# Optimization experiments

Hardware: AMD Instinct MI355X
Metric: run time of the kernel (lower is better)

The kernel has to match this reference:

```python
import jax, jax.numpy as jnp
import numpy as np

T, B, X, H, Y, D = 512, 64, 64, 1024, 64, 2


def setup_inputs() -> dict:
    key = jax.random.key(0)
    ks = jax.random.split(key, 13)
    s = 0.02  # weight init scale
    return {
        "x": jax.random.normal(ks[0], (T, B, X), dtype=jnp.float32),
        "enc_w": jax.random.normal(ks[1], (H, X), dtype=jnp.float32) * s,
        "enc_b": jax.random.normal(ks[2], (H,), dtype=jnp.float32) * s,
        "w_ih": jax.random.normal(ks[3], (D, 3 * H, H), dtype=jnp.float32) * s,
        "w_hh": jax.random.normal(ks[4], (D, 3 * H, H), dtype=jnp.float32) * s,
        "b_ih": jax.random.normal(ks[5], (D, 3 * H), dtype=jnp.float32) * s,
        "b_hh": jax.random.normal(ks[6], (D, 3 * H), dtype=jnp.float32) * s,
        "dec_w": jax.random.normal(ks[7], (H, H), dtype=jnp.float32) * s,
        "dec_b": jax.random.normal(ks[8], (H,), dtype=jnp.float32) * s,
        "exp_w": jax.random.normal(ks[9], (Y, H), dtype=jnp.float32) * s,
        "exp_b": jax.random.normal(ks[10], (Y,), dtype=jnp.float32) * s,
        "log_w": jax.random.normal(ks[11], (Y, H), dtype=jnp.float32) * s,
        "log_b": jax.random.normal(ks[12], (Y,), dtype=jnp.float32) * s,
    }


def _gru_cell(x, h, wih, whh, bih, bhh):
    # PyTorch GRUCell semantics
    gi = x @ wih.T + bih  # [B, 3H]
    gh = h @ whh.T + bhh  # [B, 3H]
    i_r, i_z, i_n = jnp.split(gi, 3, axis=-1)
    h_r, h_z, h_n = jnp.split(gh, 3, axis=-1)
    r = jax.nn.sigmoid(i_r + h_r)
    z = jax.nn.sigmoid(i_z + h_z)
    n = jnp.tanh(i_n + r * h_n)
    return (1.0 - z) * n + z * h


def reference(x, enc_w, enc_b, w_ih, w_hh, b_ih, b_hh, dec_w, dec_b,
              exp_w, exp_b, log_w, log_b):
    depth = w_ih.shape[0]
    batch = x.shape[1]
    h0 = jnp.zeros((depth, batch, w_hh.shape[-1]), dtype=x.dtype)

    def step(h_states, x_t):
        rnn_in = jnp.tanh(x_t @ enc_w.T + enc_b)  # encoder
        new_h = []
        for i in range(depth):  # small fixed stack of structurally distinct cells
            h = _gru_cell(rnn_in, h_states[i], w_ih[i], w_hh[i], b_ih[i], b_hh[i])
            new_h.append(h)
            rnn_in = h
        rnn_out = jnp.tanh(rnn_in @ dec_w.T + dec_b)  # decoder
        mean = rnn_out @ exp_w.T + exp_b
        var = jnp.exp(rnn_out @ log_w.T + log_b)
        return jnp.stack(new_h), (mean, var)

    _, (time_mean, time_var) = jax.lax.scan(step, h0, x)
    return time_mean, time_var  # each [T, B, Y]
```

## Files before the change

kernel.cpp:

```cpp
#include <hip/hip_runtime.h>
#include <hip/hip_bf16.h>
#include <cstdint>

#define T_STEPS 512
#define BATCH   64
#define XDIM    64
#define HDIM    1024
#define YDIM    64
#define BH      (BATCH * HDIM)
#define RING_D  32

#define WBLK_BYTES   98304
#define COMBO_BYTES  24576
#define TL1_OFF      16384

typedef unsigned short ushort_t;
typedef uint32_t u32;
typedef unsigned long long u64;
typedef __attribute__((ext_vector_type(8))) short short8;
typedef __attribute__((ext_vector_type(4))) float f32x4;

__device__ __forceinline__ u32 f2bf_u(float x) {
  u32 u = __float_as_uint(x);
  return (u + 0x7fffu + ((u >> 16) & 1u)) >> 16;
}
__device__ __forceinline__ ushort_t f2bf(float x) { return (ushort_t)f2bf_u(x); }

__device__ __forceinline__ float sigm(float x) { return 1.0f / (1.0f + expf(-x)); }

__device__ __forceinline__ void st_sc32(u32* p, u32 v) {
  __hip_atomic_store(p, v, __ATOMIC_RELAXED, __HIP_MEMORY_SCOPE_AGENT);
}
__device__ __forceinline__ u32 ld_sc32(const u32* p) {
  return __hip_atomic_load((u32*)p, __ATOMIC_RELAXED, __HIP_MEMORY_SCOPE_AGENT);
}

__global__ __launch_bounds__(256) void enc_kernel(
    const float* __restrict__ x, const float* __restrict__ enc_w,
    const float* __restrict__ enc_b, ushort_t* __restrict__ enc_out)
{
  __shared__ float wlds[64 * 65];
  const int lane = threadIdx.x & 63;
  const int wv   = threadIdx.x >> 6;
  const int cb = blockIdx.x & 15;
  const int rb = blockIdx.x >> 4;
  const int j  = cb * 64 + lane;
  const int r0 = rb * 16 + wv * 4;

  const float* wsrc = enc_w + (size_t)cb * 64 * XDIM;
  for (int i = threadIdx.x; i < 4096; i += 256)
    wlds[(i >> 6) * 65 + (i & 63)] = wsrc[i];
  __syncthreads();

  const float* xr = x + (size_t)r0 * XDIM;
  float acc[4] = {0.f, 0.f, 0.f, 0.f};
#pragma unroll
  for (int k = 0; k < XDIM; k += 4) {
    const float w0 = wlds[lane * 65 + k];
    const float w1 = wlds[lane * 65 + k + 1];
    const float w2 = wlds[lane * 65 + k + 2];
    const float w3 = wlds[lane * 65 + k + 3];
#pragma unroll
    for (int rr = 0; rr < 4; ++rr) {
      const float* xp = xr + rr * XDIM + k;
      acc[rr] = fmaf(xp[3], w3, fmaf(xp[2], w2, fmaf(xp[1], w1, fmaf(xp[0], w0, acc[rr]))));
    }
  }
  const float b = enc_b[j];
#pragma unroll
  for (int rr = 0; rr < 4; ++rr)
    enc_out[(size_t)(r0 + rr) * HDIM + j] = f2bf(tanhf(acc[rr] + b));
}

__global__ __launch_bounds__(256) void wprep_kernel(
    const float* __restrict__ w_ih, const float* __restrict__ w_hh,
    ushort_t* __restrict__ wfrag)
{
  const int lane = threadIdx.x & 63;
  const int wv   = threadIdx.x >> 6;
  const int c    = blockIdx.x * 4 + wv;
  const int ko = c & 15;
  const int tl = (c >> 4) & 1;
  const int c2 = (c >> 5) & 3;
  const int bid = c >> 7;
  const int g = c2 >> 1, kh = c2 & 1;
  const int layer = bid >> 7;
  const int j0 = (bid & 127) * 8;
  const float* wsrc = (g ? w_hh : w_ih) + (size_t)layer * 3 * HDIM * HDIM;

  if (tl == 0) {
    const int col = lane & 15, kgrp = lane >> 4;
    const int k = kh * 512 + ko * 32 + kgrp * 8;
    const int row = (col < 8) ? (j0 + col) : (HDIM + j0 + col - 8);
    const float* src = wsrc + (size_t)row * HDIM + k;
    short8 v;
#pragma unroll
    for (int e = 0; e < 8; ++e) v[e] = (short)f2bf(src[e]);
    const size_t byte = (size_t)bid * WBLK_BYTES + c2 * COMBO_BYTES + ko * 1024 + lane * 16;
    *(short8*)((char*)wfrag + byte) = v;
  } else if (lane < 32) {
    const int kgrp = lane >> 3, col = lane & 7;
    const int k = kh * 512 + ko * 32 + kgrp * 8;
    const int row = 2 * HDIM + j0 + col;
    const float* src = wsrc + (size_t)row * HDIM + k;
    short8 v;
#pragma unroll
    for (int e = 0; e < 8; ++e) v[e] = (short)f2bf(src[e]);
    const size_t byte = (size_t)bid * WBLK_BYTES + c2 * COMBO_BYTES + TL1_OFF + ko * 512 + lane * 16;
    *(short8*)((char*)wfrag + byte) = v;
  }
}

__global__ __launch_bounds__(256) void wprep2_kernel(
    const float* __restrict__ dec_w, const float* __restrict__ exp_w,
    const float* __restrict__ log_w,
    ushort_t* __restrict__ dwfrag, ushort_t* __restrict__ hwfrag)
{
  const int lane = threadIdx.x & 63;
  const int wv   = threadIdx.x >> 6;
  const int c    = blockIdx.x * 4 + wv;
  short8 v;
  if (c < 2048) {
    const int nt = c >> 5, kc = c & 31;
    const int row = nt * 16 + (lane & 15);
    const int k   = kc * 32 + (lane >> 4) * 8;
    const float* src = dec_w + (size_t)row * HDIM + k;
#pragma unroll
    for (int e = 0; e < 8; ++e) v[e] = (short)f2bf(src[e]);
    *(short8*)(dwfrag + (size_t)c * 512 + lane * 8) = v;
  } else {
    const int c2 = c - 2048;
    const int nt = c2 >> 5, kc = c2 & 31;
    const int row = nt * 16 + (lane & 15);
    const int k   = kc * 32 + (lane >> 4) * 8;
    const float* src = (row < 64) ? (exp_w + (size_t)row * HDIM + k)
                                  : (log_w + (size_t)(row - 64) * HDIM + k);
#pragma unroll
    for (int e = 0; e < 8; ++e) v[e] = (short)f2bf(src[e]);
    *(short8*)(hwfrag + (size_t)c2 * 512 + lane * 8) = v;
  }
}

__device__ __forceinline__ void group_bar(u32* flags, u32* rel, int gbid,
                                          bool leader, u32 tag) {
  const int tid = threadIdx.x;
  __syncthreads();
  if (tid == 0) st_sc32(flags + (size_t)gbid * 64, tag);
  if (leader) {
    if (tid < 128) {
      u32* fp = flags + (size_t)tid * 64;
      while (ld_sc32(fp) < tag) __builtin_amdgcn_s_sleep(1);
    }
    __syncthreads();
    if (tid == 0) st_sc32(rel, tag);
  } else {
    if (tid == 0) {
      while (ld_sc32(rel) < tag) __builtin_amdgcn_s_sleep(1);
    }
    __syncthreads();
  }
}

__global__ __launch_bounds__(512, 1) void rnn_persist(
    const ushort_t* __restrict__ ench1,
    const ushort_t* __restrict__ wfrag,
    const float* __restrict__ b_ih, const float* __restrict__ b_hh,
    ushort_t* __restrict__ h0ring,
    ushort_t* __restrict__ h1ring,
    ushort_t* __restrict__ h1_all,
    u32* __restrict__ l0_flags, u32* __restrict__ l1_flags,
    u32* __restrict__ l0_rel,   u32* __restrict__ l1_rel)
{
  extern __shared__ char smem[];
  float* lds_part = (float*)(smem + WBLK_BYTES);

  const int tid  = threadIdx.x;
  const int lane = tid & 63;
  const int wid  = tid >> 6;
  const int bid  = blockIdx.x;
  const int layer = bid >> 7;
  const int j0    = (bid & 127) * 8;
  const int mp = wid & 1, g = (wid >> 1) & 1, kh = wid >> 2;
  const int col = lane & 15, kgrp = lane >> 4;
  const bool isL1 = (layer == 1);
  const int gbid = bid & 127;
  const bool leader = (gbid == 0);

  {
    const uint4* src = (const uint4*)((const char*)wfrag + (size_t)bid * WBLK_BYTES);
    uint4* dst = (uint4*)smem;
#pragma unroll 4
    for (int i = tid; i < WBLK_BYTES / 16; i += 512) dst[i] = src[i];
  }

  const int c2 = g * 2 + kh;
  const char* w0 = smem + c2 * COMBO_BYTES + lane * 16;
  const char* w1 = smem + c2 * COMBO_BYTES + TL1_OFF + (kgrp * 8 + (col & 7)) * 16;

  float bA = 0.f, bB = 0.f, bC = 0.f;
  {
    const float* bi = b_ih + layer * 3 * HDIM;
    const float* bh = b_hh + layer * 3 * HDIM;
    if (col < 8) {
      const int j = j0 + col;
      bA = bi[j] + bh[j];
      bB = bi[2 * HDIM + j];
      bC = bh[2 * HDIM + j];
    } else {
      const int j = j0 + col - 8;
      bA = bi[HDIM + j] + bh[HDIM + j];
    }
  }

  f32x4 hp = {0.f, 0.f, 0.f, 0.f};

  __syncthreads();

  for (int i = 0; i < T_STEPS; ++i) {
    if (isL1) {
      if (tid == 0) {
        while (ld_sc32(l0_rel) < (u32)(i + 1)) __builtin_amdgcn_s_sleep(1);
      }
    } else if (i >= RING_D) {
      if (tid == 0) {
        while (ld_sc32(l1_rel) < (u32)(i - RING_D + 1)) __builtin_amdgcn_s_sleep(1);
      }
    }
    __syncthreads();

    const ushort_t* A1 = isL1 ? (h0ring + (size_t)(i & (RING_D - 1)) * BH)
                              : (ench1 + (size_t)i * BH);
    const ushort_t* A2 = isL1 ? (h1ring + (size_t)((i - 1) & (RING_D - 1)) * BH)
                              : (h0ring + (size_t)((i - 1) & (RING_D - 1)) * BH);
    const ushort_t* A = g ? A2 : A1;
    const ushort_t* Arow0 = A + (size_t)(mp * 32 + col) * HDIM + kh * 512 + kgrp * 8;
    const ushort_t* Arow1 = Arow0 + 16 * HDIM;

    f32x4 acc00 = {0,0,0,0}, acc01 = {0,0,0,0}, acc10 = {0,0,0,0}, acc11 = {0,0,0,0};
#pragma unroll
    for (int ko = 0; ko < 16; ++ko) {
      const short8 a0 = *(const short8*)(Arow0 + ko * 32);
      const short8 a1 = *(const short8*)(Arow1 + ko * 32);
      const short8 b0 = *(const short8*)(w0 + ko * 1024);
      const short8 b1 = *(const short8*)(w1 + ko * 512);
      acc00 = __builtin_amdgcn_mfma_f32_16x16x32_bf16(a0, b0, acc00, 0, 0, 0);
      acc01 = __builtin_amdgcn_mfma_f32_16x16x32_bf16(a0, b1, acc01, 0, 0, 0);
      acc10 = __builtin_amdgcn_mfma_f32_16x16x32_bf16(a1, b0, acc10, 0, 0, 0);
      acc11 = __builtin_amdgcn_mfma_f32_16x16x32_bf16(a1, b1, acc11, 0, 0, 0);
    }
    const int base = (wid * 4) * 256 + lane * 4;
    *(f32x4*)&lds_part[base      ] = acc00;
    *(f32x4*)&lds_part[base + 256] = acc01;
    *(f32x4*)&lds_part[base + 512] = acc10;
    *(f32x4*)&lds_part[base + 768] = acc11;

    __syncthreads();

    if (wid < 4) {
      const int m = wid, mpe = m >> 1, ime = m & 1;
      const int i00 = ((0 * 4 + 0 * 2 + mpe) * 4 + ime * 2);
      const int i01 = ((1 * 4 + 0 * 2 + mpe) * 4 + ime * 2);
      const int i10 = ((0 * 4 + 1 * 2 + mpe) * 4 + ime * 2);
      const int i11 = ((1 * 4 + 1 * 2 + mpe) * 4 + ime * 2);
      const int lo = lane * 4;
      f32x4 girz = *(f32x4*)&lds_part[i00 * 256 + lo] + *(f32x4*)&lds_part[i01 * 256 + lo];
      f32x4 gin  = *(f32x4*)&lds_part[(i00 + 1) * 256 + lo] + *(f32x4*)&lds_part[(i01 + 1) * 256 + lo];
      f32x4 ghrz = *(f32x4*)&lds_part[i10 * 256 + lo] + *(f32x4*)&lds_part[i11 * 256 + lo];
      f32x4 ghn  = *(f32x4*)&lds_part[(i10 + 1) * 256 + lo] + *(f32x4*)&lds_part[(i11 + 1) * 256 + lo];

      ushort_t* hdst = isL1 ? (h1ring + (size_t)(i & (RING_D - 1)) * BH)
                            : (h0ring + (size_t)(i & (RING_D - 1)) * BH);
      ushort_t* hall = isL1 ? (h1_all + (size_t)i * BH) : (ushort_t*)0;

#pragma unroll
      for (int e = 0; e < 4; ++e) {
        const float rz = sigm(girz[e] + ghrz[e] + bA);
        const float nv = tanhf(gin[e] + bB + rz * (ghn[e] + bC));
        const float zv = __shfl_xor(rz, 8);
        const int b = m * 16 + kgrp * 4 + e;
        float h = 0.f;
        if (col < 8) {
          h = (1.f - zv) * nv + zv * hp[e];
          hp[e] = h;
        }
        const u32 hb = f2bf_u(h);
        const u32 pb = (u32)__shfl_xor((int)hb, 1);
        if (col < 8 && (col & 1) == 0) {
          const u32 pack = hb | (pb << 16);
          st_sc32((u32*)(hdst + b * HDIM + j0 + col), pack);
          if (hall) st_sc32((u32*)(hall + b * HDIM + j0 + col), pack);
        }
      }
    }

    if (isL1) group_bar(l1_flags, l1_rel, gbid, leader, (u32)(i + 1));
    else      group_bar(l0_flags, l0_rel, gbid, leader, (u32)(i + 1));
  }
}

#define AST 1032
__global__ __launch_bounds__(512, 1) void dechead_kernel(
    const ushort_t* __restrict__ h1_all,
    const ushort_t* __restrict__ dwfrag, const ushort_t* __restrict__ hwfrag,
    const float* __restrict__ dec_b, const float* __restrict__ exp_b,
    const float* __restrict__ log_b, float* __restrict__ out)
{
  extern __shared__ char smem2[];
  ushort_t* Alds = (ushort_t*)smem2;
  ushort_t* Rlds = Alds + 32 * AST;

  const int tid  = threadIdx.x;
  const int lane = tid & 63;
  const int wv   = tid >> 6;
  const int base = blockIdx.x * 32;

  {
    const uint4* src = (const uint4*)(h1_all + (size_t)base * HDIM);
#pragma unroll
    for (int ii = 0; ii < 8; ++ii) {
      const int idx = ii * 512 + tid;
      const int row = idx >> 7;
      const int k   = (idx & 127) * 8;
      *(uint4*)(Alds + row * AST + k) = src[idx];
    }
  }
  __syncthreads();

  f32x4 acc[8][2];
#pragma unroll
  for (int t = 0; t < 8; ++t) { acc[t][0] = (f32x4){0,0,0,0}; acc[t][1] = (f32x4){0,0,0,0}; }

  const int r0 = lane & 15, kg = lane >> 4;
  const int nt0 = wv * 8;
#pragma unroll 1
  for (int t = 0; t < 8; ++t) {
    const ushort_t* bsrc = dwfrag + (size_t)(nt0 + t) * 32 * 512 + lane * 8;
    f32x4 c0 = acc[t][0], c1 = acc[t][1];
#pragma unroll
    for (int kc = 0; kc < 32; ++kc) {
      const short8 b  = *(const short8*)(bsrc + kc * 512);
      const short8 a0 = *(const short8*)(Alds + r0 * AST + kc * 32 + kg * 8);
      const short8 a1 = *(const short8*)(Alds + (16 + r0) * AST + kc * 32 + kg * 8);
      c0 = __builtin_amdgcn_mfma_f32_16x16x32_bf16(a0, b, c0, 0, 0, 0);
      c1 = __builtin_amdgcn_mfma_f32_16x16x32_bf16(a1, b, c1, 0, 0, 0);
    }
    acc[t][0] = c0; acc[t][1] = c1;
  }

#pragma unroll
  for (int t = 0; t < 8; ++t) {
    const int colc = (nt0 + t) * 16 + r0;
    const float db = dec_b[colc];
#pragma unroll
    for (int m = 0; m < 2; ++m) {
      const f32x4 v = acc[t][m];
#pragma unroll
      for (int e = 0; e < 4; ++e) {
        const int row = m * 16 + kg * 4 + e;
        Rlds[row * AST + colc] = (ushort_t)f2bf_u(tanhf(v[e] + db));
      }
    }
  }
  __syncthreads();

  f32x4 h0a = {0,0,0,0}, h1a = {0,0,0,0};
  {
    const ushort_t* bsrc = hwfrag + (size_t)wv * 32 * 512 + lane * 8;
#pragma unroll
    for (int kc = 0; kc < 32; ++kc) {
      const short8 b  = *(const short8*)(bsrc + kc * 512);
      const short8 a0 = *(const short8*)(Rlds + r0 * AST + kc * 32 + kg * 8);
      const short8 a1 = *(const short8*)(Rlds + (16 + r0) * AST + kc * 32 + kg * 8);
      h0a = __builtin_amdgcn_mfma_f32_16x16x32_bf16(a0, b, h0a, 0, 0, 0);
      h1a = __builtin_amdgcn_mfma_f32_16x16x32_bf16(a1, b, h1a, 0, 0, 0);
    }
  }
  const int y = wv * 16 + r0;
  if (wv < 4) {
    const float eb = exp_b[y];
#pragma unroll
    for (int m = 0; m < 2; ++m) {
      const f32x4 v = (m == 0) ? h0a : h1a;
#pragma unroll
      for (int e = 0; e < 4; ++e) {
        const int row = m * 16 + kg * 4 + e;
        out[(size_t)(base + row) * YDIM + y] = v[e] + eb;
      }
    }
  } else {
    const int yv = y - 64;
    const float lb = log_b[yv];
#pragma unroll
    for (int m = 0; m < 2; ++m) {
      const f32x4 v = (m == 0) ? h0a : h1a;
#pragma unroll
      for (int e = 0; e < 4; ++e) {
        const int row = m * 16 + kg * 4 + e;
        out[(size_t)(T_STEPS * BATCH * YDIM) + (size_t)(base + row) * YDIM + yv] = expf(v[e] + lb);
      }
    }
  }
}

extern "C" void kernel_launch(void* const* d_in, const int* in_sizes, int n_in,
                              void* d_out, int out_size, void* d_ws, size_t ws_size,
                              hipStream_t stream) {
  (void)in_sizes; (void)n_in; (void)out_size; (void)ws_size;
  const float* x     = (const float*)d_in[0];
  const float* enc_w = (const float*)d_in[1];
  const float* enc_b = (const float*)d_in[2];
  const float* w_ih  = (const float*)d_in[3];
  const float* w_hh  = (const float*)d_in[4];
  const float* b_ih  = (const float*)d_in[5];
  const float* b_hh  = (const float*)d_in[6];
  const float* dec_w = (const float*)d_in[7];
  const float* dec_b = (const float*)d_in[8];
  const float* exp_w = (const float*)d_in[9];
  const float* exp_b = (const float*)d_in[10];
  const float* log_w = (const float*)d_in[11];
  const float* log_b = (const float*)d_in[12];
  float* out = (float*)d_out;

  char* ws = (char*)d_ws;
  u32*      l0f     = (u32*)ws;
  u32*      l1f     = (u32*)(ws + 32768);
  u32*      l0r     = (u32*)(ws + 65536);
  u32*      l1r     = (u32*)(ws + 65792);
  ushort_t* wfrag   = (ushort_t*)(ws + 2097152);
  ushort_t* h0ring  = (ushort_t*)(ws + 27262976);
  ushort_t* h1ring  = (ushort_t*)(ws + 31457280);
  ushort_t* ench1   = (ushort_t*)(ws + 35651584);
  ushort_t* dwfrag  = (ushort_t*)(ws + 102760448);
  ushort_t* hwfrag  = (ushort_t*)(ws + 104857600);

  hipMemsetAsync(ws, 0, 66048, stream);
  hipMemsetAsync(ws + 27262976, 0, 8388608, stream);

  enc_kernel<<<32768, 256, 0, stream>>>(x, enc_w, enc_b, ench1);
  wprep_kernel<<<8192, 256, 0, stream>>>(w_ih, w_hh, wfrag);
  wprep2_kernel<<<576, 256, 0, stream>>>(dec_w, exp_w, log_w, dwfrag, hwfrag);

  {
    static int lds_opted = 0;
    if (!lds_opted) {
      hipFuncSetAttribute((const void*)rnn_persist,
                          hipFuncAttributeMaxDynamicSharedMemorySize, 131072);
      hipFuncSetAttribute((const void*)dechead_kernel,
                          hipFuncAttributeMaxDynamicSharedMemorySize, 2 * 32 * AST * 2);
      lds_opted = 1;
    }
    void* args[11];
    args[0]  = (void*)&ench1;
    args[1]  = (void*)&wfrag;
    args[2]  = (void*)&b_ih;
    args[3]  = (void*)&b_hh;
    args[4]  = (void*)&h0ring;
    args[5]  = (void*)&h1ring;
    args[6]  = (void*)&ench1;
    args[7]  = (void*)&l0f;
    args[8]  = (void*)&l1f;
    args[9]  = (void*)&l0r;
    args[10] = (void*)&l1r;
    hipLaunchCooperativeKernel((const void*)rnn_persist, dim3(256), dim3(512),
                               args, 131072, stream);
  }

  dechead_kernel<<<1024, 512, 2 * 32 * AST * 2, stream>>>(
      ench1, dwfrag, hwfrag, dec_b, exp_b, log_b, out);
}
```

Measured before the change: 5.984 ms.

## Replace leader-based group barrier with distributed flag polling and prefetch A early

Removes the two-level leader/release barrier. Each block now publishes a packed per-step flag, and consumers poll all 128 producer flags directly with 128-bit sc1 loads spread over 32 threads. The input-projection operand (g==0, which does not depend on the previous step) is loaded into registers before waiting on the recurrence flags, so that load overlaps the synchronization wait. The K loop is split into halves gated by explicit vmcnt waits. This shortens the critical path per timestep at the cost of more polling traffic, a large register array (32 uint4), and reliance on inline asm and relaxed memory ordering.

```diff
diff --git a/kernel.cpp b/kernel.cpp
--- a/kernel.cpp
+++ b/kernel.cpp
@@ -20,6 +20,8 @@
 typedef __attribute__((ext_vector_type(8))) short short8;
 typedef __attribute__((ext_vector_type(4))) float f32x4;
 
+union U4S8 { uint4 u; short8 s; };
+
 __device__ __forceinline__ u32 f2bf_u(float x) {
   u32 u = __float_as_uint(x);
   return (u + 0x7fffu + ((u >> 16) & 1u)) >> 16;
@@ -31,8 +33,22 @@
 __device__ __forceinline__ void st_sc32(u32* p, u32 v) {
   __hip_atomic_store(p, v, __ATOMIC_RELAXED, __HIP_MEMORY_SCOPE_AGENT);
 }
-__device__ __forceinline__ u32 ld_sc32(const u32* p) {
-  return __hip_atomic_load((u32*)p, __ATOMIC_RELAXED, __HIP_MEMORY_SCOPE_AGENT);
+
+__device__ __forceinline__ uint4 ld_g128(const ushort_t* p) {
+  uint4 r;
+  asm volatile("global_load_dwordx4 %0, %1, off" : "=v"(r) : "v"(p));
+  return r;
+}
+
+__device__ __forceinline__ int flags_ok(const u32* p, u32 tag) {
+  uint4 f;
+  asm volatile("global_load_dwordx4 %0, %1, off sc1\n\ts_waitcnt vmcnt(0)"
+               : "=v"(f) : "v"(p) : "memory");
+  return (f.x >= tag) && (f.y >= tag) && (f.z >= tag) && (f.w >= tag);
+}
+__device__ __forceinline__ void poll4(const u32* flags, int t, u32 tag) {
+  const u32* p = flags + 4 * t;
+  while (!flags_ok(p, tag)) __builtin_amdgcn_s_sleep(1);
 }
 
 __global__ __launch_bounds__(256) void enc_kernel(
@@ -141,26 +157,6 @@
   }
 }
 
-__device__ __forceinline__ void group_bar(u32* flags, u32* rel, int gbid,
-                                          bool leader, u32 tag) {
-  const int tid = threadIdx.x;
-  __syncthreads();
-  if (tid == 0) st_sc32(flags + (size_t)gbid * 64, tag);
-  if (leader) {
-    if (tid < 128) {
-      u32* fp = flags + (size_t)tid * 64;
-      while (ld_sc32(fp) < tag) __builtin_amdgcn_s_sleep(1);
-    }
-    __syncthreads();
-    if (tid == 0) st_sc32(rel, tag);
-  } else {
-    if (tid == 0) {
-      while (ld_sc32(rel) < tag) __builtin_amdgcn_s_sleep(1);
-    }
-    __syncthreads();
-  }
-}
-
 __global__ __launch_bounds__(512, 1) void rnn_persist(
     const ushort_t* __restrict__ ench1,
     const ushort_t* __restrict__ wfrag,
@@ -168,8 +164,7 @@
     ushort_t* __restrict__ h0ring,
     ushort_t* __restrict__ h1ring,
     ushort_t* __restrict__ h1_all,
-    u32* __restrict__ l0_flags, u32* __restrict__ l1_flags,
-    u32* __restrict__ l0_rel,   u32* __restrict__ l1_rel)
+    u32* __restrict__ l0_flags, u32* __restrict__ l1_flags)
 {
   extern __shared__ char smem[];
   float* lds_part = (float*)(smem + WBLK_BYTES);
@@ -184,7 +179,7 @@
   const int col = lane & 15, kgrp = lane >> 4;
   const bool isL1 = (layer == 1);
   const int gbid = bid & 127;
-  const bool leader = (gbid == 0);
+  u32* ownf = isL1 ? l1_flags : l0_flags;
 
   {
     const uint4* src = (const uint4*)((const char*)wfrag + (size_t)bid * WBLK_BYTES);
@@ -218,15 +213,9 @@
 
   for (int i = 0; i < T_STEPS; ++i) {
     if (isL1) {
-      if (tid == 0) {
-        while (ld_sc32(l0_rel) < (u32)(i + 1)) __builtin_amdgcn_s_sleep(1);
-      }
-    } else if (i >= RING_D) {
-      if (tid == 0) {
-        while (ld_sc32(l1_rel) < (u32)(i - RING_D + 1)) __builtin_amdgcn_s_sleep(1);
-      }
-    }
-    __syncthreads();
+      if (tid < 32) poll4(l0_flags, tid, (u32)(i + 1));
+      __syncthreads();
+    }
 
     const ushort_t* A1 = isL1 ? (h0ring + (size_t)(i & (RING_D - 1)) * BH)
                               : (ench1 + (size_t)i * BH);
@@ -236,18 +225,55 @@
     const ushort_t* Arow0 = A + (size_t)(mp * 32 + col) * HDIM + kh * 512 + kgrp * 8;
     const ushort_t* Arow1 = Arow0 + 16 * HDIM;
 
+    uint4 areg[32];
+    if (g == 0) {
+#pragma unroll
+      for (int ko = 0; ko < 16; ++ko) {
+        areg[2 * ko]     = ld_g128(Arow0 + ko * 32);
+        areg[2 * ko + 1] = ld_g128(Arow1 + ko * 32);
+      }
+    }
+
+    if (tid < 32) {
+      poll4(ownf, tid, (u32)i);
+      if (!isL1 && i >= RING_D) poll4(l1_flags, tid, (u32)(i - RING_D + 1));
+    }
+    __syncthreads();
+
+    if (g == 1) {
+#pragma unroll
+      for (int ko = 0; ko < 16; ++ko) {
+        areg[2 * ko]     = ld_g128(Arow0 + ko * 32);
+        areg[2 * ko + 1] = ld_g128(Arow1 + ko * 32);
+      }
+    }
+
     f32x4 acc00 = {0,0,0,0}, acc01 = {0,0,0,0}, acc10 = {0,0,0,0}, acc11 = {0,0,0,0};
-#pragma unroll
-    for (int ko = 0; ko < 16; ++ko) {
-      const short8 a0 = *(const short8*)(Arow0 + ko * 32);
-      const short8 a1 = *(const short8*)(Arow1 + ko * 32);
+    asm volatile("s_waitcnt vmcnt(16)" ::: "memory");
+    __builtin_amdgcn_sched_barrier(0);
+#pragma unroll
+    for (int ko = 0; ko < 8; ++ko) {
       const short8 b0 = *(const short8*)(w0 + ko * 1024);
       const short8 b1 = *(const short8*)(w1 + ko * 512);
-      acc00 = __builtin_amdgcn_mfma_f32_16x16x32_bf16(a0, b0, acc00, 0, 0, 0);
-      acc01 = __builtin_amdgcn_mfma_f32_16x16x32_bf16(a0, b1, acc01, 0, 0, 0);
-      acc10 = __builtin_amdgcn_mfma_f32_16x16x32_bf16(a1, b0, acc10, 0, 0, 0);
-      acc11 = __builtin_amdgcn_mfma_f32_16x16x32_bf16(a1, b1, acc11, 0, 0, 0);
-    }
+      U4S8 a0, a1; a0.u = areg[2 * ko]; a1.u = areg[2 * ko + 1];
+      acc00 = __builtin_amdgcn_mfma_f32_16x16x32_bf16(a0.s, b0, acc00, 0, 0, 0);
+      acc01 = __builtin_amdgcn_mfma_f32_16x16x32_bf16(a0.s, b1, acc01, 0, 0, 0);
+      acc10 = __builtin_amdgcn_mfma_f32_16x16x32_bf16(a1.s, b0, acc10, 0, 0, 0);
+      acc11 = __builtin_amdgcn_mfma_f32_16x16x32_bf16(a1.s, b1, acc11, 0, 0, 0);
+    }
+    asm volatile("s_waitcnt vmcnt(0)" ::: "memory");
+    __builtin_amdgcn_sched_barrier(0);
+#pragma unroll
+    for (int ko = 8; ko < 16; ++ko) {
+      const short8 b0 = *(const short8*)(w0 + ko * 1024);
+      const short8 b1 = *(const short8*)(w1 + ko * 512);
+      U4S8 a0, a1; a0.u = areg[2 * ko]; a1.u = areg[2 * ko + 1];
+      acc00 = __builtin_amdgcn_mfma_f32_16x16x32_bf16(a0.s, b0, acc00, 0, 0, 0);
+      acc01 = __builtin_amdgcn_mfma_f32_16x16x32_bf16(a0.s, b1, acc01, 0, 0, 0);
+      acc10 = __builtin_amdgcn_mfma_f32_16x16x32_bf16(a1.s, b0, acc10, 0, 0, 0);
+      acc11 = __builtin_amdgcn_mfma_f32_16x16x32_bf16(a1.s, b1, acc11, 0, 0, 0);
+    }
+
     const int base = (wid * 4) * 256 + lane * 4;
     *(f32x4*)&lds_part[base      ] = acc00;
     *(f32x4*)&lds_part[base + 256] = acc01;
@@ -293,8 +319,8 @@
       }
     }
 
-    if (isL1) group_bar(l1_flags, l1_rel, gbid, leader, (u32)(i + 1));
-    else      group_bar(l0_flags, l0_rel, gbid, leader, (u32)(i + 1));
+    __syncthreads();
+    if (tid == 0) st_sc32(ownf + gbid, (u32)(i + 1));
   }
 }
 
@@ -423,9 +449,7 @@
 
   char* ws = (char*)d_ws;
   u32*      l0f     = (u32*)ws;
-  u32*      l1f     = (u32*)(ws + 32768);
-  u32*      l0r     = (u32*)(ws + 65536);
-  u32*      l1r     = (u32*)(ws + 65792);
+  u32*      l1f     = (u32*)(ws + 4096);
   ushort_t* wfrag   = (ushort_t*)(ws + 2097152);
   ushort_t* h0ring  = (ushort_t*)(ws + 27262976);
   ushort_t* h1ring  = (ushort_t*)(ws + 31457280);
@@ -433,7 +457,7 @@
   ushort_t* dwfrag  = (ushort_t*)(ws + 102760448);
   ushort_t* hwfrag  = (ushort_t*)(ws + 104857600);
 
-  hipMemsetAsync(ws, 0, 66048, stream);
+  hipMemsetAsync(ws, 0, 8192, stream);
   hipMemsetAsync(ws + 27262976, 0, 8388608, stream);
 
   enc_kernel<<<32768, 256, 0, stream>>>(x, enc_w, enc_b, ench1);
@@ -449,18 +473,16 @@
                           hipFuncAttributeMaxDynamicSharedMemorySize, 2 * 32 * AST * 2);
       lds_opted = 1;
     }
-    void* args[11];
-    args[0]  = (void*)&ench1;
-    args[1]  = (void*)&wfrag;
-    args[2]  = (void*)&b_ih;
-    args[3]  = (void*)&b_hh;
-    args[4]  = (void*)&h0ring;
-    args[5]  = (void*)&h1ring;
-    args[6]  = (void*)&ench1;
-    args[7]  = (void*)&l0f;
-    args[8]  = (void*)&l1f;
-    args[9]  = (void*)&l0r;
-    args[10] = (void*)&l1r;
+    void* args[9];
+    args[0] = (void*)&ench1;
+    args[1] = (void*)&wfrag;
+    args[2] = (void*)&b_ih;
+    args[3] = (void*)&b_hh;
+    args[4] = (void*)&h0ring;
+    args[5] = (void*)&h1ring;
+    args[6] = (void*)&ench1;
+    args[7] = (void*)&l0f;
+    args[8] = (void*)&l1f;
     hipLaunchCooperativeKernel((const void*)rnn_persist, dim3(256), dim3(512),
                                args, 131072, stream);
   }
```

New measurement: 5.573 ms. 1.07x faster.
